# Optimization experiments

Hardware: AMD Instinct MI355X
Metric: run time of the kernel (lower is better)

Reference implementation:

```python
import jax, jax.numpy as jnp
import numpy as np

GRID_W, GRID_H = 4, 4          # num_splits = (4, 4) -> 16 experts
N = 524288                     # number of sample points
IN_DIM, HID, OUT = 2, 256, 3   # per-expert MLP: 2 -> 256 -> 3


def setup_inputs() -> dict:
    key = jax.random.key(0)
    k_s, k_w1, k_w2 = jax.random.split(key, 3)
    E = GRID_W * GRID_H
    samples = jax.random.uniform(k_s, (N, IN_DIM), dtype=jnp.float32)
    W1 = jax.random.normal(k_w1, (E, IN_DIM, HID), dtype=jnp.float32) * (1.0 / np.sqrt(IN_DIM))
    b1 = jnp.zeros((E, HID), dtype=jnp.float32)
    W2 = jax.random.normal(k_w2, (E, HID, OUT), dtype=jnp.float32) * (1.0 / np.sqrt(HID))
    b2 = jnp.zeros((E, OUT), dtype=jnp.float32)
    return {"samples": samples, "W1": W1, "b1": b1, "W2": W2, "b2": b2}


def _grid_inds(samples):
    # i, j = floor(samples[:, d] * n).clip(0, n-1); inds = j * w + i
    i = jnp.clip(jnp.floor(samples[:, 0] * GRID_W), 0, GRID_W - 1)
    j = jnp.clip(jnp.floor(samples[:, 1] * GRID_H), 0, GRID_H - 1)
    return (j * GRID_W + i).astype(jnp.int32)  # [N]


def reference(samples, W1, b1, W2, b2):
    inds = _grid_inds(samples)                     # [N] expert id per sample
    E = W1.shape[0]
    out = jnp.zeros((samples.shape[0], W2.shape[-1]), dtype=samples.dtype)
    # Dense dispatch: loop over the small fixed set of experts (16) and
    # select each sample's own expert output via the routing mask. Same
    # math as torch's features[inds == i] gather + scatter combine.
    for e in range(E):
        h = jax.nn.relu(samples @ W1[e] + b1[e])   # [N, HID]
        y = h @ W2[e] + b2[e]                      # [N, OUT]
        out = jnp.where((inds == e)[:, None], y, out)
    return out
```

## Files before the change

kernel.cpp:

```cpp
#include <hip/hip_runtime.h>

typedef _Float16 h2 __attribute__((ext_vector_type(2)));

#define GRID_W 4
#define GRID_H 4
#define NEXP   16
#define HID    256
#define TPB    1024
#define S      2
#define SAMP   (TPB * S)
#define NWAVE  (TPB / 64)
#define WPE    1536
#define GR     192
#define MAXENT 32

#define NSLOT  (SAMP + GR)
#define OFFB_I (NSLOT * 8)
#define LDS_BYTES (OFFB_I + 4 * (16 + 17 + 17 + 3 * MAXENT + 1))

__global__ __launch_bounds__(256) void convert_kernel(
    const float* __restrict__ W1, const float* __restrict__ b1,
    const float* __restrict__ W2, _Float16* __restrict__ wsW) {
    int t = blockIdx.x * 256 + threadIdx.x;
    int e = t >> 8, k = t & 255;
    _Float16* dst = wsW + e * WPE;
    dst[k]        = (_Float16)W1[e * 512 + k];
    dst[256 + k]  = (_Float16)W1[e * 512 + 256 + k];
    dst[512 + k]  = (_Float16)b1[e * 256 + k];
    dst[768 + k]  = (_Float16)W2[e * 768 + 3 * k];
    dst[1024 + k] = (_Float16)W2[e * 768 + 3 * k + 1];
    dst[1280 + k] = (_Float16)W2[e * 768 + 3 * k + 2];
}

union H8 { float4 f; h2 p[4]; };

template<int M>
__device__ __forceinline__ void mlp_pass(const float4* __restrict__ W4,
                                         const h2* px2, const h2* py2,
                                         float (*y)[3]) {
#pragma unroll 4
    for (int b = 0; b < 32; ++b) {
        H8 wa, wb, bb, u0, u1, u2;
        wa.f = W4[b];
        wb.f = W4[32 + b];
        bb.f = W4[64 + b];
        u0.f = W4[96 + b];
        u1.f = W4[128 + b];
        u2.f = W4[160 + b];
#pragma unroll
        for (int j = 0; j < 4; ++j) {
#pragma unroll
            for (int s = 0; s < M; ++s) {
                h2 h = __builtin_elementwise_fma(px2[s], wa.p[j],
                       __builtin_elementwise_fma(py2[s], wb.p[j], bb.p[j]));
                h2 z = (h2)(_Float16)0.0f;
                h = __builtin_elementwise_max(h, z);
#if __has_builtin(__builtin_amdgcn_fdot2)
                y[s][0] = __builtin_amdgcn_fdot2(h, u0.p[j], y[s][0], false);
                y[s][1] = __builtin_amdgcn_fdot2(h, u1.p[j], y[s][1], false);
                y[s][2] = __builtin_amdgcn_fdot2(h, u2.p[j], y[s][2], false);
#else
                y[s][0] += (float)h.x * (float)u0.p[j].x + (float)h.y * (float)u0.p[j].y;
                y[s][1] += (float)h.x * (float)u1.p[j].x + (float)h.y * (float)u1.p[j].y;
                y[s][2] += (float)h.x * (float)u2.p[j].x + (float)h.y * (float)u2.p[j].y;
#endif
            }
        }
    }
}

__global__ __launch_bounds__(TPB) void fused_smem_moe_kernel(
    const float2* __restrict__ samples,
    const _Float16* __restrict__ wsW,
    const float* __restrict__ b2,
    float* __restrict__ out, int N)
{
    extern __shared__ __align__(16) char smem[];
    int2* sSlot = (int2*)smem;
    int*  sI    = (int*)(smem + OFFB_I);
    int* sHist = sI;
    int* sOff  = sI + 16;
    int* sES   = sI + 33;
    int* sEexp = sI + 50;
    int* sEbas = sI + 50 + MAXENT;
    int* sEcnt = sI + 50 + 2 * MAXENT;
    int* sC    = sI + 50 + 3 * MAXENT;

    const int tid = threadIdx.x;
    if (tid < NEXP) sHist[tid] = 0;
    __syncthreads();

    const int base0 = blockIdx.x * SAMP;
    float px[S], py[S]; int eid[S], rank[S], gid[S]; bool act[S];
#pragma unroll
    for (int s = 0; s < S; ++s) {
        gid[s] = base0 + s * TPB + tid;
        act[s] = gid[s] < N;
        float2 p = act[s] ? samples[gid[s]] : make_float2(0.f, 0.f);
        px[s] = p.x; py[s] = p.y;
        int i = (int)(p.x * (float)GRID_W); i = i < 0 ? 0 : (i > GRID_W - 1 ? GRID_W - 1 : i);
        int j = (int)(p.y * (float)GRID_H); j = j < 0 ? 0 : (j > GRID_H - 1 ? GRID_H - 1 : j);
        eid[s] = j * GRID_W + i;
        rank[s] = act[s] ? atomicAdd(&sHist[eid[s]], 1) : 0;
    }
    __syncthreads();

    if (tid == 0) {
        int acc = 0, ec = 0;
        for (int e = 0; e < NEXP; ++e) {
            sOff[e] = acc; acc += sHist[e];
            sES[e] = ec;  ec  += (sHist[e] + GR - 1) / GR;
        }
        sOff[NEXP] = acc; sES[NEXP] = ec; *sC = ec;
    }
    __syncthreads();

#pragma unroll
    for (int s = 0; s < S; ++s) {
        if (act[s]) {
            union { h2 h; int i; } u;
            u.h.x = (_Float16)px[s]; u.h.y = (_Float16)py[s];
            int2 v; v.x = u.i; v.y = gid[s];
            sSlot[sOff[eid[s]] + rank[s]] = v;
        }
    }
    int C = *sC;
    if (tid < C) {
        int e = 0;
        while (tid >= sES[e + 1]) ++e;
        int j = tid - sES[e];
        sEexp[tid] = e;
        sEbas[tid] = sOff[e] + j * GR;
        sEcnt[tid] = min(GR, sHist[e] - j * GR);
    }
    __syncthreads();

    const int lane = tid & 63, wv = tid >> 6;
    for (int c = wv; c < C; c += NWAVE) {
        int e   = __builtin_amdgcn_readfirstlane(sEexp[c]);
        int bas = __builtin_amdgcn_readfirstlane(sEbas[c]);
        int cnt = __builtin_amdgcn_readfirstlane(sEcnt[c]);
        const float4* W4 = (const float4*)(wsW + e * WPE);
        float b20 = b2[3 * e], b21 = b2[3 * e + 1], b22 = b2[3 * e + 2];
        int m = (cnt + 63) >> 6;

        h2 px2[3], py2[3]; int qg[3]; float yy[3][3];
#pragma unroll
        for (int s = 0; s < 3; ++s) {
            if (s < m) {
                int2 v = sSlot[bas + s * 64 + lane];
                union { int i; h2 h; } u; u.i = v.x;
                px2[s].x = u.h.x; px2[s].y = u.h.x;
                py2[s].x = u.h.y; py2[s].y = u.h.y;
                qg[s] = v.y;
                yy[s][0] = b20; yy[s][1] = b21; yy[s][2] = b22;
            }
        }

        if (m == 3)      mlp_pass<3>(W4, px2, py2, yy);
        else if (m == 2) mlp_pass<2>(W4, px2, py2, yy);
        else             mlp_pass<1>(W4, px2, py2, yy);

#pragma unroll
        for (int s = 0; s < 3; ++s) {
            if (s < m && s * 64 + lane < cnt) {
                int i3 = 3 * qg[s];
                out[i3 + 0] = yy[s][0];
                out[i3 + 1] = yy[s][1];
                out[i3 + 2] = yy[s][2];
            }
        }
    }
}

extern "C" void kernel_launch(void* const* d_in, const int* in_sizes, int n_in,
                              void* d_out, int out_size, void* d_ws, size_t ws_size,
                              hipStream_t stream) {
    const float* samples = (const float*)d_in[0];
    const float* W1      = (const float*)d_in[1];
    const float* b1      = (const float*)d_in[2];
    const float* W2      = (const float*)d_in[3];
    const float* b2      = (const float*)d_in[4];
    float* out = (float*)d_out;

    const int N = in_sizes[0] / 2;
    _Float16* wsW = (_Float16*)d_ws;

    convert_kernel<<<NEXP, 256, 0, stream>>>(W1, b1, W2, wsW);

    const int nblocks = (N + SAMP - 1) / SAMP;
    fused_smem_moe_kernel<<<nblocks, TPB, LDS_BYTES, stream>>>(
        (const float2*)samples, wsW, b2, out, N);
}
```

Measured before the change: 85.04 us.

## Split fused MoE kernel into global sort pass and per-wave MLP kernel

Replaces the single fused kernel, which binned samples in LDS and then had each 1024-thread block loop its waves over expert chunks, with two kernels. A sort kernel buckets samples by expert into a global slot array and writes 64-sample work entries. A separate 256-thread MLP kernel then assigns one wave per entry. This is meant to fix load imbalance and the low occupancy of the large LDS-bound blocks. In exchange it adds a kernel launch, a global round trip for the slots, and padding entries whose waves exit early. It also drops the multi-chunk register reuse of each weight load across up to three sample groups.

```diff
diff --git a/kernel.cpp b/kernel.cpp
--- a/kernel.cpp
+++ b/kernel.cpp
@@ -6,17 +6,16 @@
 #define GRID_H 4
 #define NEXP   16
 #define HID    256
-#define TPB    1024
+#define STPB   1024
 #define S      2
-#define SAMP   (TPB * S)
-#define NWAVE  (TPB / 64)
+#define SAMP   (STPB * S)
 #define WPE    1536
-#define GR     192
-#define MAXENT 32
+#define MAXE   48
+#define MTPB   256
+#define MWAVES (MTPB / 64)
 
-#define NSLOT  (SAMP + GR)
-#define OFFB_I (NSLOT * 8)
-#define LDS_BYTES (OFFB_I + 4 * (16 + 17 + 17 + 3 * MAXENT + 1))
+#define WSOFF_ENT  65536
+#define WSOFF_SLOT (4u << 20)
 
 __global__ __launch_bounds__(256) void convert_kernel(
     const float* __restrict__ W1, const float* __restrict__ b1,
@@ -32,59 +31,12 @@
     dst[1280 + k] = (_Float16)W2[e * 768 + 3 * k + 2];
 }
 
-union H8 { float4 f; h2 p[4]; };
-
-template<int M>
-__device__ __forceinline__ void mlp_pass(const float4* __restrict__ W4,
-                                         const h2* px2, const h2* py2,
-                                         float (*y)[3]) {
-#pragma unroll 4
-    for (int b = 0; b < 32; ++b) {
-        H8 wa, wb, bb, u0, u1, u2;
-        wa.f = W4[b];
-        wb.f = W4[32 + b];
-        bb.f = W4[64 + b];
-        u0.f = W4[96 + b];
-        u1.f = W4[128 + b];
-        u2.f = W4[160 + b];
-#pragma unroll
-        for (int j = 0; j < 4; ++j) {
-#pragma unroll
-            for (int s = 0; s < M; ++s) {
-                h2 h = __builtin_elementwise_fma(px2[s], wa.p[j],
-                       __builtin_elementwise_fma(py2[s], wb.p[j], bb.p[j]));
-                h2 z = (h2)(_Float16)0.0f;
-                h = __builtin_elementwise_max(h, z);
-#if __has_builtin(__builtin_amdgcn_fdot2)
-                y[s][0] = __builtin_amdgcn_fdot2(h, u0.p[j], y[s][0], false);
-                y[s][1] = __builtin_amdgcn_fdot2(h, u1.p[j], y[s][1], false);
-                y[s][2] = __builtin_amdgcn_fdot2(h, u2.p[j], y[s][2], false);
-#else
-                y[s][0] += (float)h.x * (float)u0.p[j].x + (float)h.y * (float)u0.p[j].y;
-                y[s][1] += (float)h.x * (float)u1.p[j].x + (float)h.y * (float)u1.p[j].y;
-                y[s][2] += (float)h.x * (float)u2.p[j].x + (float)h.y * (float)u2.p[j].y;
-#endif
-            }
-        }
-    }
-}
-
-__global__ __launch_bounds__(TPB) void fused_smem_moe_kernel(
-    const float2* __restrict__ samples,
-    const _Float16* __restrict__ wsW,
-    const float* __restrict__ b2,
-    float* __restrict__ out, int N)
-{
-    extern __shared__ __align__(16) char smem[];
-    int2* sSlot = (int2*)smem;
-    int*  sI    = (int*)(smem + OFFB_I);
-    int* sHist = sI;
-    int* sOff  = sI + 16;
-    int* sES   = sI + 33;
-    int* sEexp = sI + 50;
-    int* sEbas = sI + 50 + MAXENT;
-    int* sEcnt = sI + 50 + 2 * MAXENT;
-    int* sC    = sI + 50 + 3 * MAXENT;
+__global__ __launch_bounds__(STPB) void sort_kernel(
+    const float2* __restrict__ samples, int N,
+    int2* __restrict__ slots, int4* __restrict__ entries) {
+    __shared__ int sHist[NEXP];
+    __shared__ int sOff[NEXP + 1];
+    __shared__ int sES[NEXP + 1];
 
     const int tid = threadIdx.x;
     if (tid < NEXP) sHist[tid] = 0;
@@ -94,7 +46,7 @@
     float px[S], py[S]; int eid[S], rank[S], gid[S]; bool act[S];
 #pragma unroll
     for (int s = 0; s < S; ++s) {
-        gid[s] = base0 + s * TPB + tid;
+        gid[s] = base0 + s * STPB + tid;
         act[s] = gid[s] < N;
         float2 p = act[s] ? samples[gid[s]] : make_float2(0.f, 0.f);
         px[s] = p.x; py[s] = p.y;
@@ -109,9 +61,9 @@
         int acc = 0, ec = 0;
         for (int e = 0; e < NEXP; ++e) {
             sOff[e] = acc; acc += sHist[e];
-            sES[e] = ec;  ec  += (sHist[e] + GR - 1) / GR;
+            sES[e] = ec;  ec  += (sHist[e] + 63) >> 6;
         }
-        sOff[NEXP] = acc; sES[NEXP] = ec; *sC = ec;
+        sOff[NEXP] = acc; sES[NEXP] = ec;
     }
     __syncthreads();
 
@@ -121,55 +73,81 @@
             union { h2 h; int i; } u;
             u.h.x = (_Float16)px[s]; u.h.y = (_Float16)py[s];
             int2 v; v.x = u.i; v.y = gid[s];
-            sSlot[sOff[eid[s]] + rank[s]] = v;
+            slots[base0 + sOff[eid[s]] + rank[s]] = v;
         }
     }
-    int C = *sC;
-    if (tid < C) {
-        int e = 0;
-        while (tid >= sES[e + 1]) ++e;
-        int j = tid - sES[e];
-        sEexp[tid] = e;
-        sEbas[tid] = sOff[e] + j * GR;
-        sEcnt[tid] = min(GR, sHist[e] - j * GR);
+    if (tid < MAXE) {
+        int C = sES[NEXP];
+        int4 ent; ent.x = 0; ent.y = base0; ent.z = 0; ent.w = 0;
+        if (tid < C) {
+            int e = 0;
+            while (tid >= sES[e + 1]) ++e;
+            int j = tid - sES[e];
+            ent.x = e;
+            ent.y = base0 + sOff[e] + j * 64;
+            ent.z = min(64, sHist[e] - j * 64);
+        }
+        entries[blockIdx.x * MAXE + tid] = ent;
     }
-    __syncthreads();
+}
 
-    const int lane = tid & 63, wv = tid >> 6;
-    for (int c = wv; c < C; c += NWAVE) {
-        int e   = __builtin_amdgcn_readfirstlane(sEexp[c]);
-        int bas = __builtin_amdgcn_readfirstlane(sEbas[c]);
-        int cnt = __builtin_amdgcn_readfirstlane(sEcnt[c]);
-        const float4* W4 = (const float4*)(wsW + e * WPE);
-        float b20 = b2[3 * e], b21 = b2[3 * e + 1], b22 = b2[3 * e + 2];
-        int m = (cnt + 63) >> 6;
+union H8 { float4 f; h2 p[4]; };
 
-        h2 px2[3], py2[3]; int qg[3]; float yy[3][3];
+__global__ __launch_bounds__(MTPB) void mlp_kernel(
+    const _Float16* __restrict__ wsW, const int2* __restrict__ slots,
+    const int4* __restrict__ entries, const float* __restrict__ b2,
+    float* __restrict__ out, int NE) {
+    const int g = blockIdx.x * MWAVES + (threadIdx.x >> 6);
+    const int lane = threadIdx.x & 63;
+    if (g >= NE) return;
+
+    int4 ent = entries[g];
+    int e   = __builtin_amdgcn_readfirstlane(ent.x);
+    int bas = __builtin_amdgcn_readfirstlane(ent.y);
+    int cnt = __builtin_amdgcn_readfirstlane(ent.z);
+    if (cnt == 0) return;
+
+    int2 v = slots[bas + lane];
+    union { int i; h2 h; } u; u.i = v.x;
+    h2 px2; px2.x = u.h.x; px2.y = u.h.x;
+    h2 py2; py2.x = u.h.y; py2.y = u.h.y;
+    int qg = v.y;
+
+    float y0 = b2[3 * e], y1 = b2[3 * e + 1], y2 = b2[3 * e + 2];
+    const float4* W4 = (const float4*)(wsW + e * WPE);
+
+#pragma unroll 2
+    for (int b = 0; b < 32; ++b) {
+        H8 wa, wb, bb, u0, u1, u2;
+        wa.f = W4[b];
+        wb.f = W4[32 + b];
+        bb.f = W4[64 + b];
+        u0.f = W4[96 + b];
+        u1.f = W4[128 + b];
+        u2.f = W4[160 + b];
 #pragma unroll
-        for (int s = 0; s < 3; ++s) {
-            if (s < m) {
-                int2 v = sSlot[bas + s * 64 + lane];
-                union { int i; h2 h; } u; u.i = v.x;
-                px2[s].x = u.h.x; px2[s].y = u.h.x;
-                py2[s].x = u.h.y; py2[s].y = u.h.y;
-                qg[s] = v.y;
-                yy[s][0] = b20; yy[s][1] = b21; yy[s][2] = b22;
-            }
+        for (int j = 0; j < 4; ++j) {
+            h2 h = __builtin_elementwise_fma(px2, wa.p[j],
+                   __builtin_elementwise_fma(py2, wb.p[j], bb.p[j]));
+            h2 z = (h2)(_Float16)0.0f;
+            h = __builtin_elementwise_max(h, z);
+#if __has_builtin(__builtin_amdgcn_fdot2)
+            y0 = __builtin_amdgcn_fdot2(h, u0.p[j], y0, false);
+            y1 = __builtin_amdgcn_fdot2(h, u1.p[j], y1, false);
+            y2 = __builtin_amdgcn_fdot2(h, u2.p[j], y2, false);
+#else
+            y0 += (float)h.x * (float)u0.p[j].x + (float)h.y * (float)u0.p[j].y;
+            y1 += (float)h.x * (float)u1.p[j].x + (float)h.y * (float)u1.p[j].y;
+            y2 += (float)h.x * (float)u2.p[j].x + (float)h.y * (float)u2.p[j].y;
+#endif
         }
+    }
 
-        if (m == 3)      mlp_pass<3>(W4, px2, py2, yy);
-        else if (m == 2) mlp_pass<2>(W4, px2, py2, yy);
-        else             mlp_pass<1>(W4, px2, py2, yy);
-
-#pragma unroll
-        for (int s = 0; s < 3; ++s) {
-            if (s < m && s * 64 + lane < cnt) {
-                int i3 = 3 * qg[s];
-                out[i3 + 0] = yy[s][0];
-                out[i3 + 1] = yy[s][1];
-                out[i3 + 2] = yy[s][2];
-            }
-        }
+    if (lane < cnt) {
+        int i3 = 3 * qg;
+        out[i3 + 0] = y0;
+        out[i3 + 1] = y1;
+        out[i3 + 2] = y2;
     }
 }
 
@@ -184,11 +162,16 @@
     float* out = (float*)d_out;
 
     const int N = in_sizes[0] / 2;
-    _Float16* wsW = (_Float16*)d_ws;
+    _Float16* wsW   = (_Float16*)d_ws;
+    int4*     ents  = (int4*)((char*)d_ws + WSOFF_ENT);
+    int2*     slots = (int2*)((char*)d_ws + WSOFF_SLOT);
 
     convert_kernel<<<NEXP, 256, 0, stream>>>(W1, b1, W2, wsW);
 
-    const int nblocks = (N + SAMP - 1) / SAMP;
-    fused_smem_moe_kernel<<<nblocks, TPB, LDS_BYTES, stream>>>(
-        (const float2*)samples, wsW, b2, out, N);
+    const int nsb = (N + SAMP - 1) / SAMP;
+    sort_kernel<<<nsb, STPB, 0, stream>>>((const float2*)samples, N, slots, ents);
+
+    const int NE = nsb * MAXE;
+    mlp_kernel<<<(NE + MWAVES - 1) / MWAVES, MTPB, 0, stream>>>(
+        wsW, slots, ents, b2, out, NE);
 }
```

After: 91.85 us. 8.0% more time.

## Software-pipeline weight loads, vectorize sample reads, and reshape blocks to 512x4

Applied to the files above, without the earlier changes.

The per-expert MLP loop now prefetches the next 32-element weight batch into registers while computing the current one, so global/L2 latency overlaps the FMA/fdot2 math. Each thread loads two samples at once with a float4 read instead of two float2 reads. The block shrinks to 512 threads with 4 samples per thread, and launch bounds ask for 4 blocks per CU. The prefetch doubles the live weight registers and the new shape changes per-block chunk counts, which may affect occupancy and load balance. The compile-time fallback for missing fdot2 is also dropped.

```diff
diff --git a/kernel.cpp b/kernel.cpp
--- a/kernel.cpp
+++ b/kernel.cpp
@@ -6,8 +6,8 @@
 #define GRID_H 4
 #define NEXP   16
 #define HID    256
-#define TPB    1024
-#define S      2
+#define TPB    512
+#define S      4
 #define SAMP   (TPB * S)
 #define NWAVE  (TPB / 64)
 #define WPE    1536
@@ -33,44 +33,53 @@
 }
 
 union H8 { float4 f; h2 p[4]; };
+struct WBatch { H8 wa, wb, bb, u0, u1, u2; };
+
+__device__ __forceinline__ WBatch wload(const float4* __restrict__ W4, int b) {
+    WBatch w;
+    w.wa.f = W4[b];
+    w.wb.f = W4[32 + b];
+    w.bb.f = W4[64 + b];
+    w.u0.f = W4[96 + b];
+    w.u1.f = W4[128 + b];
+    w.u2.f = W4[160 + b];
+    return w;
+}
+
+template<int M>
+__device__ __forceinline__ void wmath(const WBatch& w, const h2* px2,
+                                      const h2* py2, float (*y)[3]) {
+#pragma unroll
+    for (int j = 0; j < 4; ++j) {
+#pragma unroll
+        for (int s = 0; s < M; ++s) {
+            h2 h = __builtin_elementwise_fma(px2[s], w.wa.p[j],
+                   __builtin_elementwise_fma(py2[s], w.wb.p[j], w.bb.p[j]));
+            h2 z = (h2)(_Float16)0.0f;
+            h = __builtin_elementwise_max(h, z);
+            y[s][0] = __builtin_amdgcn_fdot2(h, w.u0.p[j], y[s][0], false);
+            y[s][1] = __builtin_amdgcn_fdot2(h, w.u1.p[j], y[s][1], false);
+            y[s][2] = __builtin_amdgcn_fdot2(h, w.u2.p[j], y[s][2], false);
+        }
+    }
+}
 
 template<int M>
 __device__ __forceinline__ void mlp_pass(const float4* __restrict__ W4,
                                          const h2* px2, const h2* py2,
                                          float (*y)[3]) {
-#pragma unroll 4
-    for (int b = 0; b < 32; ++b) {
-        H8 wa, wb, bb, u0, u1, u2;
-        wa.f = W4[b];
-        wb.f = W4[32 + b];
-        bb.f = W4[64 + b];
-        u0.f = W4[96 + b];
-        u1.f = W4[128 + b];
-        u2.f = W4[160 + b];
-#pragma unroll
-        for (int j = 0; j < 4; ++j) {
-#pragma unroll
-            for (int s = 0; s < M; ++s) {
-                h2 h = __builtin_elementwise_fma(px2[s], wa.p[j],
-                       __builtin_elementwise_fma(py2[s], wb.p[j], bb.p[j]));
-                h2 z = (h2)(_Float16)0.0f;
-                h = __builtin_elementwise_max(h, z);
-#if __has_builtin(__builtin_amdgcn_fdot2)
-                y[s][0] = __builtin_amdgcn_fdot2(h, u0.p[j], y[s][0], false);
-                y[s][1] = __builtin_amdgcn_fdot2(h, u1.p[j], y[s][1], false);
-                y[s][2] = __builtin_amdgcn_fdot2(h, u2.p[j], y[s][2], false);
-#else
-                y[s][0] += (float)h.x * (float)u0.p[j].x + (float)h.y * (float)u0.p[j].y;
-                y[s][1] += (float)h.x * (float)u1.p[j].x + (float)h.y * (float)u1.p[j].y;
-                y[s][2] += (float)h.x * (float)u2.p[j].x + (float)h.y * (float)u2.p[j].y;
-#endif
-            }
-        }
-    }
-}
-
-__global__ __launch_bounds__(TPB) void fused_smem_moe_kernel(
-    const float2* __restrict__ samples,
+    WBatch cur = wload(W4, 0);
+#pragma unroll 2
+    for (int b = 0; b < 31; ++b) {
+        WBatch nxt = wload(W4, b + 1);
+        wmath<M>(cur, px2, py2, y);
+        cur = nxt;
+    }
+    wmath<M>(cur, px2, py2, y);
+}
+
+__global__ __launch_bounds__(TPB, 4) void fused_moe_kernel(
+    const float4* __restrict__ samples4,
     const _Float16* __restrict__ wsW,
     const float* __restrict__ b2,
     float* __restrict__ out, int N)
@@ -93,15 +102,23 @@
     const int base0 = blockIdx.x * SAMP;
     float px[S], py[S]; int eid[S], rank[S], gid[S]; bool act[S];
 #pragma unroll
-    for (int s = 0; s < S; ++s) {
-        gid[s] = base0 + s * TPB + tid;
-        act[s] = gid[s] < N;
-        float2 p = act[s] ? samples[gid[s]] : make_float2(0.f, 0.f);
-        px[s] = p.x; py[s] = p.y;
-        int i = (int)(p.x * (float)GRID_W); i = i < 0 ? 0 : (i > GRID_W - 1 ? GRID_W - 1 : i);
-        int j = (int)(p.y * (float)GRID_H); j = j < 0 ? 0 : (j > GRID_H - 1 ? GRID_H - 1 : j);
-        eid[s] = j * GRID_W + i;
-        rank[s] = act[s] ? atomicAdd(&sHist[eid[s]], 1) : 0;
+    for (int r = 0; r < S / 2; ++r) {
+        int f4i = (base0 >> 1) + r * TPB + tid;
+        int g = 2 * (r * TPB + tid);
+        bool in = base0 + g < N;
+        float4 v = in ? samples4[f4i] : make_float4(0.f, 0.f, 0.f, 0.f);
+#pragma unroll
+        for (int h = 0; h < 2; ++h) {
+            int s = 2 * r + h;
+            gid[s] = base0 + g + h;
+            act[s] = in;
+            float x = h ? v.z : v.x, yv = h ? v.w : v.y;
+            px[s] = x; py[s] = yv;
+            int i = (int)(x  * (float)GRID_W); i = i < 0 ? 0 : (i > GRID_W - 1 ? GRID_W - 1 : i);
+            int j = (int)(yv * (float)GRID_H); j = j < 0 ? 0 : (j > GRID_H - 1 ? GRID_H - 1 : j);
+            eid[s] = j * GRID_W + i;
+            rank[s] = act[s] ? atomicAdd(&sHist[eid[s]], 1) : 0;
+        }
     }
     __syncthreads();
 
@@ -189,6 +206,6 @@
     convert_kernel<<<NEXP, 256, 0, stream>>>(W1, b1, W2, wsW);
 
     const int nblocks = (N + SAMP - 1) / SAMP;
-    fused_smem_moe_kernel<<<nblocks, TPB, LDS_BYTES, stream>>>(
-        (const float2*)samples, wsW, b2, out, N);
-}
+    fused_moe_kernel<<<nblocks, TPB, LDS_BYTES, stream>>>(
+        (const float4*)samples, wsW, b2, out, N);
+}
```

Measured after the change: 91.36 us. 1.07x slower.
